# Kernel optimization log

Hardware: AMD Instinct MI355X
Metric: run time of the kernel (lower is better)

Reference implementation:

```python
import jax, jax.numpy as jnp
import numpy as np

T, H, I, E, Z = 4096, 1024, 512, 64, 16   # tokens, hidden, intermediate, routed experts, zero experts
TOP_K = 2
SCALE = 1.5        # routed_scaling_factor
CAP = 320


def setup_inputs() -> dict:
    key = jax.random.key(0)
    k1, k2, k3, k4, k5 = jax.random.split(key, 5)
    return {
        "hidden_states": jax.random.normal(k1, (T, H), dtype=jnp.float32),
        "router_w": jax.random.normal(k2, (E + Z, H), dtype=jnp.float32) * 0.02,
        "correction_bias": jnp.zeros((E + Z,), dtype=jnp.float32),
        "w_gate": jax.random.normal(k3, (E, H, I), dtype=jnp.float32) * 0.02,
        "w_up": jax.random.normal(k4, (E, H, I), dtype=jnp.float32) * 0.02,
        "w_down": jax.random.normal(k5, (E, I, H), dtype=jnp.float32) * 0.02,
    }


def _moe_forward(hidden_states, router_w, correction_bias, w_gate, w_up, w_down):
    n_tok = hidden_states.shape[0]
    # ---- Router (fp32 gemm) ----
    logits = hidden_states @ router_w.T                      # [T, E+Z]
    scores = jax.nn.sigmoid(logits)                          # DeepSeek-V3-style sigmoid gating
    biased = scores + correction_bias[None, :]
    _, top_idx = jax.lax.top_k(biased, TOP_K)                # [T, K] selection on biased scores
    top_w = jnp.take_along_axis(scores, top_idx, axis=-1)    # weights from unbiased scores, no renorm

    # ---- Zero (identity) experts: ids >= E return the input token ----
    is_zero = top_idx >= E                                   # [T, K]
    zero_out = (top_w * is_zero).sum(-1, keepdims=True) * hidden_states

    # ---- Routed expert dispatch (capacity-based grouped GEMM) ----
    flat_e = jnp.where(is_zero, 0, top_idx).reshape(-1)      # [T*K]
    flat_w = jnp.where(is_zero, 0.0, top_w).reshape(-1)      # [T*K]
    routed_mask = (~is_zero).reshape(-1)
    oh = jax.nn.one_hot(flat_e, E, dtype=jnp.int32) * routed_mask[:, None].astype(jnp.int32)
    pos = (jnp.cumsum(oh, axis=0) * oh).sum(-1) - 1          # rank within expert; -1 for zero-expert slots
    valid = (pos >= 0) & (pos < CAP)
    pos_c = jnp.where(valid, pos, CAP)                       # overflow/zero slots -> spill row CAP
    x_rep = jnp.repeat(hidden_states, TOP_K, axis=0)         # [T*K, H]
    buf = jnp.zeros((E, CAP + 1, hidden_states.shape[1]), dtype=hidden_states.dtype)
    buf = buf.at[flat_e, pos_c].set(x_rep)[:, :CAP]          # [E, CAP, H]

    # ---- Grouped SwiGLU experts ----
    g = jax.nn.silu(jnp.einsum('ech,ehi->eci', buf, w_gate)) * jnp.einsum('ech,ehi->eci', buf, w_up)
    out_e = jnp.einsum('eci,eih->ech', g, w_down)            # [E, CAP, H]

    # ---- Combine ----
    pos_g = jnp.where(valid, pos, 0)
    y = out_e[flat_e, pos_g] * (flat_w * valid)[:, None]     # [T*K, H]
    routed = y.reshape(n_tok, TOP_K, -1).sum(1)

    return (routed + zero_out) * SCALE                       # routed_scaling_factor applied on output


def reference(hidden_states, router_w, correction_bias, w_gate, w_up, w_down):
    return _moe_forward(hidden_states, router_w, correction_bias, w_gate, w_up, w_down)
```

## Files before the change

### kernel.cpp

```cpp
#include <hip/hip_runtime.h>
#include <hip/hip_bf16.h>
#include <stdint.h>


#define T_TOK 4096
#define HDIM  1024
#define IDIM  512
#define NE    64
#define NEZ   80
#define CAPE  320
#define SCALEF 1.5f

typedef __attribute__((ext_vector_type(8))) short bf16x8;
typedef __attribute__((ext_vector_type(4))) float floatx4;

static __device__ __forceinline__ unsigned short f2bf(float f) {
    unsigned int x = __float_as_uint(f);
    x += 0x7fffu + ((x >> 16) & 1u);
    return (unsigned short)(x >> 16);
}
static __device__ __forceinline__ float bf2f(unsigned short u) {
    return __uint_as_float(((unsigned int)u) << 16);
}
static __device__ __forceinline__ uint4 pack8(const float* f) {
    uint4 v;
    asm("v_cvt_pk_bf16_f32 %0, %1, %2" : "=v"(v.x) : "v"(f[0]), "v"(f[1]));
    asm("v_cvt_pk_bf16_f32 %0, %1, %2" : "=v"(v.y) : "v"(f[2]), "v"(f[3]));
    asm("v_cvt_pk_bf16_f32 %0, %1, %2" : "=v"(v.z) : "v"(f[4]), "v"(f[5]));
    asm("v_cvt_pk_bf16_f32 %0, %1, %2" : "=v"(v.w) : "v"(f[6]), "v"(f[7]));
    return v;
}
static __device__ __forceinline__ uint2 pack4(float4 f) {
    uint2 v;
    asm("v_cvt_pk_bf16_f32 %0, %1, %2" : "=v"(v.x) : "v"(f.x), "v"(f.y));
    asm("v_cvt_pk_bf16_f32 %0, %1, %2" : "=v"(v.y) : "v"(f.z), "v"(f.w));
    return v;
}

__global__ __launch_bounds__(256) void router_kernel(
    const float* __restrict__ hidden, const float* __restrict__ rw,
    const float* __restrict__ bias, int* __restrict__ cnt,
    int* __restrict__ slot_tok, float* __restrict__ w_routed,
    float* __restrict__ zc)
{
    __shared__ float sc[8][NEZ];
    __shared__ float sbias[NEZ];
    const int tid = threadIdx.x;
    const int w = tid >> 6, lane = tid & 63;
    const int t0 = blockIdx.x * 8 + w * 2;

    if (tid < NEZ) sbias[tid] = bias[tid];

    float4 xr[2][4];
#pragma unroll
    for (int tt = 0; tt < 2; ++tt)
#pragma unroll
        for (int j4 = 0; j4 < 4; ++j4)
            xr[tt][j4] = *(const float4*)&hidden[(size_t)(t0 + tt) * HDIM + lane * 16 + j4 * 4];

    for (int eb = 0; eb < NEZ; eb += 16) {
        float acc[2][16];
#pragma unroll
        for (int tt = 0; tt < 2; ++tt)
#pragma unroll
            for (int ee = 0; ee < 16; ++ee) acc[tt][ee] = 0.f;

#pragma unroll
        for (int ee = 0; ee < 16; ++ee) {
            const float* r = rw + (size_t)(eb + ee) * HDIM + lane * 16;
#pragma unroll
            for (int j4 = 0; j4 < 4; ++j4) {
                float4 rv = *(const float4*)&r[j4 * 4];
                acc[0][ee] += xr[0][j4].x * rv.x + xr[0][j4].y * rv.y
                            + xr[0][j4].z * rv.z + xr[0][j4].w * rv.w;
                acc[1][ee] += xr[1][j4].x * rv.x + xr[1][j4].y * rv.y
                            + xr[1][j4].z * rv.z + xr[1][j4].w * rv.w;
            }
        }
#pragma unroll
        for (int off = 32; off > 0; off >>= 1)
#pragma unroll
            for (int tt = 0; tt < 2; ++tt)
#pragma unroll
                for (int ee = 0; ee < 16; ++ee)
                    acc[tt][ee] += __shfl_xor(acc[tt][ee], off);

        if (lane == 0) {
#pragma unroll
            for (int tt = 0; tt < 2; ++tt)
#pragma unroll
                for (int ee = 0; ee < 16; ++ee)
                    sc[w * 2 + tt][eb + ee] = 1.f / (1.f + __expf(-acc[tt][ee]));
        }
    }
    __syncthreads();

    if (tid < 8) {
        const int t = blockIdx.x * 8 + tid;
        float b1 = -1e30f, b2 = -1e30f; int i1 = 0, i2 = 0;
        for (int e = 0; e < NEZ; ++e) {
            float b = sc[tid][e] + sbias[e];
            if (b > b1) { b2 = b1; i2 = i1; b1 = b; i1 = e; }
            else if (b > b2) { b2 = b; i2 = e; }
        }
        float z = 0.f;
        int idx2[2] = { i1, i2 };
        for (int k = 0; k < 2; ++k) {
            int e = idx2[k];
            float wgt = sc[tid][e];
            float wr = 0.f;
            if (e >= NE) {
                z += wgt;
            } else {
                int pos = atomicAdd(&cnt[e], 1);
                if (pos < CAPE) { slot_tok[e * CAPE + pos] = t * 2 + k; wr = wgt; }
            }
            w_routed[t * 2 + k] = wr;
        }
        zc[t] = z;
    }
}

#define GU_BG 2048
#define GU_BU 4096
__global__ __launch_bounds__(256, 4) void gateup_kernel(
    const float* __restrict__ hidden,
    const float* __restrict__ w_gate, const float* __restrict__ w_up,
    const int* __restrict__ cnt, const int* __restrict__ slot_tok,
    unsigned short* __restrict__ gbuf)
{
    const int e  = blockIdx.x;
    const int n0 = blockIdx.y * 64;
    const int m0 = blockIdx.z * 64;
    int cnt_e = cnt[e]; if (cnt_e > CAPE) cnt_e = CAPE;
    if (m0 >= cnt_e) return;

    __shared__ unsigned short lds[6144];
    __shared__ int sTok[64];

    const int tid = threadIdx.x;
    const int lane = tid & 63, wid = tid >> 6;
    const int ml = lane & 15, quad = lane >> 4;
    const int wm = wid >> 1, wn = wid & 1;

    if (tid < 64) {
        int r = m0 + tid;
        sTok[tid] = (r < cnt_e) ? (slot_tok[e * CAPE + r] >> 1) : 0;
    }
    __syncthreads();

    const int ak4 = tid & 7;
    const float* ha[2];
    int aoff[2];
#pragma unroll
    for (int p = 0; p < 2; ++p) {
        int arow = (tid >> 3) + 32 * p;
        aoff[p] = (arow >> 4) * 512 + ((ak4 >> 1) * 16 + (arow & 15)) * 8 + (ak4 & 1) * 4;
        ha[p] = hidden + (size_t)sTok[arow] * HDIM + ak4 * 4;
    }
    const int bn = tid & 63, bq = tid >> 6;
    const int boff = (bn >> 4) * 512 + (bq * 16 + (bn & 15)) * 8;

    const size_t ebase = (size_t)e * HDIM * IDIM;
    const float* wg_p = w_gate + ebase + (size_t)(bq * 8) * IDIM + n0 + bn;
    const float* wu_p = w_up   + ebase + (size_t)(bq * 8) * IDIM + n0 + bn;

    float4 aR[2];
    float  gR[8], uR[8];

#pragma unroll
    for (int p = 0; p < 2; ++p) aR[p] = *(const float4*)ha[p];
#pragma unroll
    for (int jj = 0; jj < 8; ++jj) {
        gR[jj] = wg_p[(size_t)jj * IDIM];
        uR[jj] = wu_p[(size_t)jj * IDIM];
    }

    floatx4 ag[2][2], au[2][2];
#pragma unroll
    for (int mt = 0; mt < 2; ++mt)
#pragma unroll
        for (int nt = 0; nt < 2; ++nt) {
            ag[mt][nt] = (floatx4){0.f, 0.f, 0.f, 0.f};
            au[mt][nt] = (floatx4){0.f, 0.f, 0.f, 0.f};
        }

    for (int kc = 0; kc < HDIM; kc += 32) {
        {
#pragma unroll
            for (int p = 0; p < 2; ++p)
                *(uint2*)&lds[aoff[p]] = pack4(aR[p]);
            *(uint4*)&lds[GU_BG + boff] = pack8(gR);
            *(uint4*)&lds[GU_BU + boff] = pack8(uR);
        }
        __syncthreads();

        if (kc + 32 < HDIM) {
            wg_p += (size_t)32 * IDIM; wu_p += (size_t)32 * IDIM;
#pragma unroll
            for (int p = 0; p < 2; ++p) { ha[p] += 32; aR[p] = *(const float4*)ha[p]; }
#pragma unroll
            for (int jj = 0; jj < 8; ++jj) {
                gR[jj] = wg_p[(size_t)jj * IDIM];
                uR[jj] = wu_p[(size_t)jj * IDIM];
            }
        }

        bf16x8 a[2], bg[2], bu[2];
#pragma unroll
        for (int mt = 0; mt < 2; ++mt)
            a[mt] = *(const bf16x8*)&lds[(wm * 2 + mt) * 512 + lane * 8];
#pragma unroll
        for (int nt = 0; nt < 2; ++nt) {
            bg[nt] = *(const bf16x8*)&lds[GU_BG + (wn * 2 + nt) * 512 + lane * 8];
            bu[nt] = *(const bf16x8*)&lds[GU_BU + (wn * 2 + nt) * 512 + lane * 8];
        }
#pragma unroll
        for (int mt = 0; mt < 2; ++mt)
#pragma unroll
            for (int nt = 0; nt < 2; ++nt) {
                ag[mt][nt] = __builtin_amdgcn_mfma_f32_16x16x32_bf16(a[mt], bg[nt], ag[mt][nt], 0, 0, 0);
                au[mt][nt] = __builtin_amdgcn_mfma_f32_16x16x32_bf16(a[mt], bu[nt], au[mt][nt], 0, 0, 0);
            }
        __syncthreads();
    }

#pragma unroll
    for (int mt = 0; mt < 2; ++mt) {
#pragma unroll
        for (int r4 = 0; r4 < 4; ++r4) {
            int gm = m0 + wm * 32 + mt * 16 + quad * 4 + r4;
            if (gm < cnt_e) {
                unsigned short* grow = gbuf + (size_t)(e * CAPE + gm) * IDIM + n0 + wn * 32;
#pragma unroll
                for (int nt = 0; nt < 2; ++nt) {
                    float g = ag[mt][nt][r4];
                    float u = au[mt][nt][r4];
                    float s = g / (1.f + __expf(-g));
                    grow[nt * 16 + ml] = f2bf(s * u);
                }
            }
        }
    }
}

#define DN_B 2048
__global__ __launch_bounds__(256, 4) void down_kernel(
    const unsigned short* __restrict__ gbuf, const float* __restrict__ w_down,
    const int* __restrict__ cnt, const int* __restrict__ slot_tok,
    unsigned short* __restrict__ y2)
{
    const int e  = blockIdx.x;
    const int n0 = blockIdx.y * 128;
    const int m0 = blockIdx.z * 64;
    int cnt_e = cnt[e]; if (cnt_e > CAPE) cnt_e = CAPE;
    if (m0 >= cnt_e) return;

    __shared__ unsigned short lds[6144];
    __shared__ int sSlot[64];

    const int tid = threadIdx.x;
    const int lane = tid & 63, wid = tid >> 6;
    const int ml = lane & 15, quad = lane >> 4;
    const int wm = wid >> 1, wn = wid & 1;

    if (tid < 64) {
        int r = m0 + tid;
        sSlot[tid] = (r < cnt_e) ? slot_tok[e * CAPE + r] : 0;
    }
    __syncthreads();

    const int arow = tid >> 2, au8 = tid & 3;
    const int aoff = (arow >> 4) * 512 + (au8 * 16 + (arow & 15)) * 8;
    const unsigned short* gp = gbuf + (size_t)(e * CAPE + m0 + arow) * IDIM + au8 * 8;
    const int bn = tid & 127, bk = tid >> 7;
    const int boff0 = (bn >> 4) * 512 + ((bk * 2) * 16 + (bn & 15)) * 8;
    const int boff1 = boff0 + 128;
    const float* wd_p = w_down + (size_t)e * IDIM * HDIM + (size_t)(bk * 16) * HDIM + n0 + bn;

    uint4 aR;
    float bR[16];

    aR = *(const uint4*)gp;
#pragma unroll
    for (int jj = 0; jj < 16; ++jj) bR[jj] = wd_p[(size_t)jj * HDIM];

    floatx4 acc[2][4];
#pragma unroll
    for (int mt = 0; mt < 2; ++mt)
#pragma unroll
        for (int nt = 0; nt < 4; ++nt)
            acc[mt][nt] = (floatx4){0.f, 0.f, 0.f, 0.f};

    for (int kc = 0; kc < IDIM; kc += 32) {
        *(uint4*)&lds[aoff] = aR;
        *(uint4*)&lds[DN_B + boff0] = pack8(bR);
        *(uint4*)&lds[DN_B + boff1] = pack8(bR + 8);
        __syncthreads();

        if (kc + 32 < IDIM) {
            gp += 32;
            wd_p += (size_t)32 * HDIM;
            aR = *(const uint4*)gp;
#pragma unroll
            for (int jj = 0; jj < 16; ++jj) bR[jj] = wd_p[(size_t)jj * HDIM];
        }

        bf16x8 a[2], b[4];
#pragma unroll
        for (int mt = 0; mt < 2; ++mt)
            a[mt] = *(const bf16x8*)&lds[(wm * 2 + mt) * 512 + lane * 8];
#pragma unroll
        for (int nt = 0; nt < 4; ++nt)
            b[nt] = *(const bf16x8*)&lds[DN_B + (wn * 4 + nt) * 512 + lane * 8];
#pragma unroll
        for (int mt = 0; mt < 2; ++mt)
#pragma unroll
            for (int nt = 0; nt < 4; ++nt)
                acc[mt][nt] = __builtin_amdgcn_mfma_f32_16x16x32_bf16(a[mt], b[nt], acc[mt][nt], 0, 0, 0);
        __syncthreads();
    }

#pragma unroll
    for (int mt = 0; mt < 2; ++mt) {
#pragma unroll
        for (int r4 = 0; r4 < 4; ++r4) {
            int lrow = wm * 32 + mt * 16 + quad * 4 + r4;
            if (m0 + lrow < cnt_e) {
                int slot = sSlot[lrow];
                unsigned short* yrow = y2 + (size_t)slot * HDIM + n0 + wn * 64;
#pragma unroll
                for (int nt = 0; nt < 4; ++nt)
                    yrow[nt * 16 + ml] = f2bf(acc[mt][nt][r4]);
            }
        }
    }
}

__global__ __launch_bounds__(256) void combine_kernel(
    const float* __restrict__ hidden, const unsigned short* __restrict__ y2,
    const float* __restrict__ w_routed, const float* __restrict__ zc,
    float* __restrict__ out)
{
    int gid = blockIdx.x * 256 + threadIdx.x;
    int t = gid >> 8;
    int h = (gid & 255) * 4;
    float4 x = *(const float4*)(hidden + (size_t)t * HDIM + h);
    float w0 = w_routed[t * 2 + 0];
    float w1 = w_routed[t * 2 + 1];
    float z  = zc[t];
    ushort4 ya = *(const ushort4*)(y2 + (size_t)(t * 2 + 0) * HDIM + h);
    ushort4 yb = *(const ushort4*)(y2 + (size_t)(t * 2 + 1) * HDIM + h);
    float4 o;
    o.x = SCALEF * (z * x.x + w0 * bf2f(ya.x) + w1 * bf2f(yb.x));
    o.y = SCALEF * (z * x.y + w0 * bf2f(ya.y) + w1 * bf2f(yb.y));
    o.z = SCALEF * (z * x.z + w0 * bf2f(ya.z) + w1 * bf2f(yb.z));
    o.w = SCALEF * (z * x.w + w0 * bf2f(ya.w) + w1 * bf2f(yb.w));
    *(float4*)(out + (size_t)t * HDIM + h) = o;
}

#define OFF_CNT   0
#define OFF_SLOT  4096
#define OFF_WR    (OFF_SLOT + NE * CAPE * 4)
#define OFF_ZC    (OFF_WR + T_TOK * 2 * 4)
#define OFF_GBUF  (OFF_ZC + T_TOK * 4)
#define OFF_Y2    (OFF_GBUF + (size_t)NE * CAPE * IDIM * 2)

extern "C" void kernel_launch(void* const* d_in, const int* in_sizes, int n_in,
                              void* d_out, int out_size, void* d_ws, size_t ws_size,
                              hipStream_t stream) {
    const float* hidden = (const float*)d_in[0];
    const float* rw     = (const float*)d_in[1];
    const float* bias   = (const float*)d_in[2];
    const float* w_gate = (const float*)d_in[3];
    const float* w_up   = (const float*)d_in[4];
    const float* w_down = (const float*)d_in[5];
    float* out = (float*)d_out;

    char* ws = (char*)d_ws;
    int*   cnt      = (int*)(ws + OFF_CNT);
    int*   slot_tok = (int*)(ws + OFF_SLOT);
    float* w_rt     = (float*)(ws + OFF_WR);
    float* zc       = (float*)(ws + OFF_ZC);
    unsigned short* gbuf = (unsigned short*)(ws + OFF_GBUF);
    unsigned short* y2   = (unsigned short*)(ws + OFF_Y2);

    hipMemsetAsync(cnt, 0, NE * sizeof(int), stream);

    router_kernel<<<T_TOK / 8, 256, 0, stream>>>(hidden, rw, bias, cnt, slot_tok, w_rt, zc);

    gateup_kernel<<<dim3(NE, IDIM / 64, CAPE / 64), 256, 0, stream>>>(
        hidden, w_gate, w_up, cnt, slot_tok, gbuf);

    down_kernel<<<dim3(NE, HDIM / 128, CAPE / 64), 256, 0, stream>>>(
        gbuf, w_down, cnt, slot_tok, y2);

    combine_kernel<<<(T_TOK * HDIM / 4) / 256, 256, 0, stream>>>(
        hidden, y2, w_rt, zc, out);
}
```

Before: 484.8 us.

## Widen gate/up N-tile to 128 and restructure router to 16 lanes per token

The gate/up kernel now computes a 64x128 output tile per block instead of 64x64. Each gathered hidden-state tile is reused across twice as many weight columns, and the number of blocks that re-read activations is halved. Launch bounds drop to 2 blocks per SM and LDS and register use grow, which may reduce occupancy. Separately, the router now assigns 16 lanes per token and 16 tokens per block, using a shorter shuffle reduction, so router weights are read once per 16 tokens instead of once per 8.

```diff
diff --git a/kernel.cpp b/kernel.cpp
--- a/kernel.cpp
+++ b/kernel.cpp
@@ -43,60 +43,50 @@
     int* __restrict__ slot_tok, float* __restrict__ w_routed,
     float* __restrict__ zc)
 {
-    __shared__ float sc[8][NEZ];
+    __shared__ float sc[16][NEZ];
     __shared__ float sbias[NEZ];
     const int tid = threadIdx.x;
     const int w = tid >> 6, lane = tid & 63;
-    const int t0 = blockIdx.x * 8 + w * 2;
+    const int g = lane >> 4, s = lane & 15;
+    const int t = blockIdx.x * 16 + w * 4 + g;
 
     if (tid < NEZ) sbias[tid] = bias[tid];
 
-    float4 xr[2][4];
-#pragma unroll
-    for (int tt = 0; tt < 2; ++tt)
-#pragma unroll
-        for (int j4 = 0; j4 < 4; ++j4)
-            xr[tt][j4] = *(const float4*)&hidden[(size_t)(t0 + tt) * HDIM + lane * 16 + j4 * 4];
-
-    for (int eb = 0; eb < NEZ; eb += 16) {
-        float acc[2][16];
-#pragma unroll
-        for (int tt = 0; tt < 2; ++tt)
-#pragma unroll
-            for (int ee = 0; ee < 16; ++ee) acc[tt][ee] = 0.f;
-
-#pragma unroll
-        for (int ee = 0; ee < 16; ++ee) {
-            const float* r = rw + (size_t)(eb + ee) * HDIM + lane * 16;
-#pragma unroll
-            for (int j4 = 0; j4 < 4; ++j4) {
-                float4 rv = *(const float4*)&r[j4 * 4];
-                acc[0][ee] += xr[0][j4].x * rv.x + xr[0][j4].y * rv.y
-                            + xr[0][j4].z * rv.z + xr[0][j4].w * rv.w;
-                acc[1][ee] += xr[1][j4].x * rv.x + xr[1][j4].y * rv.y
-                            + xr[1][j4].z * rv.z + xr[1][j4].w * rv.w;
-            }
-        }
-#pragma unroll
-        for (int off = 32; off > 0; off >>= 1)
-#pragma unroll
-            for (int tt = 0; tt < 2; ++tt)
-#pragma unroll
-                for (int ee = 0; ee < 16; ++ee)
-                    acc[tt][ee] += __shfl_xor(acc[tt][ee], off);
-
-        if (lane == 0) {
-#pragma unroll
-            for (int tt = 0; tt < 2; ++tt)
-#pragma unroll
-                for (int ee = 0; ee < 16; ++ee)
-                    sc[w * 2 + tt][eb + ee] = 1.f / (1.f + __expf(-acc[tt][ee]));
+    float4 xr[16];
+#pragma unroll
+    for (int j = 0; j < 16; ++j)
+        xr[j] = *(const float4*)&hidden[(size_t)t * HDIM + j * 64 + s * 4];
+
+    for (int eb = 0; eb < NEZ; eb += 8) {
+        float acc[8];
+#pragma unroll
+        for (int i = 0; i < 8; ++i) acc[i] = 0.f;
+
+#pragma unroll
+        for (int j = 0; j < 16; ++j) {
+#pragma unroll
+            for (int i = 0; i < 8; ++i) {
+                float4 rv = *(const float4*)&rw[(size_t)(eb + i) * HDIM + j * 64 + s * 4];
+                acc[i] += xr[j].x * rv.x + xr[j].y * rv.y
+                        + xr[j].z * rv.z + xr[j].w * rv.w;
+            }
+        }
+#pragma unroll
+        for (int off = 8; off > 0; off >>= 1)
+#pragma unroll
+            for (int i = 0; i < 8; ++i)
+                acc[i] += __shfl_xor(acc[i], off);
+
+        if (s == 0) {
+#pragma unroll
+            for (int i = 0; i < 8; ++i)
+                sc[w * 4 + g][eb + i] = 1.f / (1.f + __expf(-acc[i]));
         }
     }
     __syncthreads();
 
-    if (tid < 8) {
-        const int t = blockIdx.x * 8 + tid;
+    if (tid < 16) {
+        const int t2 = blockIdx.x * 16 + tid;
         float b1 = -1e30f, b2 = -1e30f; int i1 = 0, i2 = 0;
         for (int e = 0; e < NEZ; ++e) {
             float b = sc[tid][e] + sbias[e];
@@ -113,29 +103,29 @@
                 z += wgt;
             } else {
                 int pos = atomicAdd(&cnt[e], 1);
-                if (pos < CAPE) { slot_tok[e * CAPE + pos] = t * 2 + k; wr = wgt; }
-            }
-            w_routed[t * 2 + k] = wr;
-        }
-        zc[t] = z;
+                if (pos < CAPE) { slot_tok[e * CAPE + pos] = t2 * 2 + k; wr = wgt; }
+            }
+            w_routed[t2 * 2 + k] = wr;
+        }
+        zc[t2] = z;
     }
 }
 
 #define GU_BG 2048
-#define GU_BU 4096
-__global__ __launch_bounds__(256, 4) void gateup_kernel(
+#define GU_BU 6144
+__global__ __launch_bounds__(256, 2) void gateup_kernel(
     const float* __restrict__ hidden,
     const float* __restrict__ w_gate, const float* __restrict__ w_up,
     const int* __restrict__ cnt, const int* __restrict__ slot_tok,
     unsigned short* __restrict__ gbuf)
 {
     const int e  = blockIdx.x;
-    const int n0 = blockIdx.y * 64;
+    const int n0 = blockIdx.y * 128;
     const int m0 = blockIdx.z * 64;
     int cnt_e = cnt[e]; if (cnt_e > CAPE) cnt_e = CAPE;
     if (m0 >= cnt_e) return;
 
-    __shared__ unsigned short lds[6144];
+    __shared__ unsigned short lds[10240];
     __shared__ int sTok[64];
 
     const int tid = threadIdx.x;
@@ -149,76 +139,76 @@
     }
     __syncthreads();
 
-    const int ak4 = tid & 7;
-    const float* ha[2];
-    int aoff[2];
-#pragma unroll
-    for (int p = 0; p < 2; ++p) {
-        int arow = (tid >> 3) + 32 * p;
-        aoff[p] = (arow >> 4) * 512 + ((ak4 >> 1) * 16 + (arow & 15)) * 8 + (ak4 & 1) * 4;
-        ha[p] = hidden + (size_t)sTok[arow] * HDIM + ak4 * 4;
-    }
-    const int bn = tid & 63, bq = tid >> 6;
-    const int boff = (bn >> 4) * 512 + (bq * 16 + (bn & 15)) * 8;
+    const int arow0 = tid >> 3, ak4 = tid & 7;
+    const int aoff0 = (arow0 >> 4) * 512 + ((ak4 >> 1) * 16 + (arow0 & 15)) * 8 + (ak4 & 1) * 4;
+    const int arow1 = arow0 + 32;
+    const int aoff1 = (arow1 >> 4) * 512 + ((ak4 >> 1) * 16 + (arow1 & 15)) * 8 + (ak4 & 1) * 4;
+    const int bn = tid & 127, bk = tid >> 7;
+    const int boff0 = (bn >> 4) * 512 + ((bk * 2) * 16 + (bn & 15)) * 8;
+    const int boff1 = boff0 + 128;
 
     const size_t ebase = (size_t)e * HDIM * IDIM;
-    const float* wg_p = w_gate + ebase + (size_t)(bq * 8) * IDIM + n0 + bn;
-    const float* wu_p = w_up   + ebase + (size_t)(bq * 8) * IDIM + n0 + bn;
+    const float* wg_p = w_gate + ebase + (size_t)(bk * 16) * IDIM + n0 + bn;
+    const float* wu_p = w_up   + ebase + (size_t)(bk * 16) * IDIM + n0 + bn;
+    const float* ha0 = hidden + (size_t)sTok[arow0] * HDIM + ak4 * 4;
+    const float* ha1 = hidden + (size_t)sTok[arow1] * HDIM + ak4 * 4;
 
     float4 aR[2];
-    float  gR[8], uR[8];
-
-#pragma unroll
-    for (int p = 0; p < 2; ++p) aR[p] = *(const float4*)ha[p];
-#pragma unroll
-    for (int jj = 0; jj < 8; ++jj) {
+    float  gR[16], uR[16];
+
+    aR[0] = *(const float4*)ha0;
+    aR[1] = *(const float4*)ha1;
+#pragma unroll
+    for (int jj = 0; jj < 16; ++jj) {
         gR[jj] = wg_p[(size_t)jj * IDIM];
         uR[jj] = wu_p[(size_t)jj * IDIM];
     }
 
-    floatx4 ag[2][2], au[2][2];
+    floatx4 ag[2][4], au[2][4];
 #pragma unroll
     for (int mt = 0; mt < 2; ++mt)
 #pragma unroll
-        for (int nt = 0; nt < 2; ++nt) {
+        for (int nt = 0; nt < 4; ++nt) {
             ag[mt][nt] = (floatx4){0.f, 0.f, 0.f, 0.f};
             au[mt][nt] = (floatx4){0.f, 0.f, 0.f, 0.f};
         }
 
     for (int kc = 0; kc < HDIM; kc += 32) {
         {
-#pragma unroll
-            for (int p = 0; p < 2; ++p)
-                *(uint2*)&lds[aoff[p]] = pack4(aR[p]);
-            *(uint4*)&lds[GU_BG + boff] = pack8(gR);
-            *(uint4*)&lds[GU_BU + boff] = pack8(uR);
+            *(uint2*)&lds[aoff0] = pack4(aR[0]);
+            *(uint2*)&lds[aoff1] = pack4(aR[1]);
+            *(uint4*)&lds[GU_BG + boff0] = pack8(gR);
+            *(uint4*)&lds[GU_BG + boff1] = pack8(gR + 8);
+            *(uint4*)&lds[GU_BU + boff0] = pack8(uR);
+            *(uint4*)&lds[GU_BU + boff1] = pack8(uR + 8);
         }
         __syncthreads();
 
         if (kc + 32 < HDIM) {
+            ha0 += 32; ha1 += 32;
             wg_p += (size_t)32 * IDIM; wu_p += (size_t)32 * IDIM;
-#pragma unroll
-            for (int p = 0; p < 2; ++p) { ha[p] += 32; aR[p] = *(const float4*)ha[p]; }
-#pragma unroll
-            for (int jj = 0; jj < 8; ++jj) {
+            aR[0] = *(const float4*)ha0;
+            aR[1] = *(const float4*)ha1;
+#pragma unroll
+            for (int jj = 0; jj < 16; ++jj) {
                 gR[jj] = wg_p[(size_t)jj * IDIM];
                 uR[jj] = wu_p[(size_t)jj * IDIM];
             }
         }
 
-        bf16x8 a[2], bg[2], bu[2];
+        bf16x8 a[2], bg[4], bu[4];
 #pragma unroll
         for (int mt = 0; mt < 2; ++mt)
             a[mt] = *(const bf16x8*)&lds[(wm * 2 + mt) * 512 + lane * 8];
 #pragma unroll
-        for (int nt = 0; nt < 2; ++nt) {
-            bg[nt] = *(const bf16x8*)&lds[GU_BG + (wn * 2 + nt) * 512 + lane * 8];
-            bu[nt] = *(const bf16x8*)&lds[GU_BU + (wn * 2 + nt) * 512 + lane * 8];
+        for (int nt = 0; nt < 4; ++nt) {
+            bg[nt] = *(const bf16x8*)&lds[GU_BG + (wn * 4 + nt) * 512 + lane * 8];
+            bu[nt] = *(const bf16x8*)&lds[GU_BU + (wn * 4 + nt) * 512 + lane * 8];
         }
 #pragma unroll
         for (int mt = 0; mt < 2; ++mt)
 #pragma unroll
-            for (int nt = 0; nt < 2; ++nt) {
+            for (int nt = 0; nt < 4; ++nt) {
                 ag[mt][nt] = __builtin_amdgcn_mfma_f32_16x16x32_bf16(a[mt], bg[nt], ag[mt][nt], 0, 0, 0);
                 au[mt][nt] = __builtin_amdgcn_mfma_f32_16x16x32_bf16(a[mt], bu[nt], au[mt][nt], 0, 0, 0);
             }
@@ -231,9 +221,9 @@
         for (int r4 = 0; r4 < 4; ++r4) {
             int gm = m0 + wm * 32 + mt * 16 + quad * 4 + r4;
             if (gm < cnt_e) {
-                unsigned short* grow = gbuf + (size_t)(e * CAPE + gm) * IDIM + n0 + wn * 32;
-#pragma unroll
-                for (int nt = 0; nt < 2; ++nt) {
+                unsigned short* grow = gbuf + (size_t)(e * CAPE + gm) * IDIM + n0 + wn * 64;
+#pragma unroll
+                for (int nt = 0; nt < 4; ++nt) {
                     float g = ag[mt][nt][r4];
                     float u = au[mt][nt][r4];
                     float s = g / (1.f + __expf(-g));
@@ -387,9 +377,9 @@
 
     hipMemsetAsync(cnt, 0, NE * sizeof(int), stream);
 
-    router_kernel<<<T_TOK / 8, 256, 0, stream>>>(hidden, rw, bias, cnt, slot_tok, w_rt, zc);
-
-    gateup_kernel<<<dim3(NE, IDIM / 64, CAPE / 64), 256, 0, stream>>>(
+    router_kernel<<<T_TOK / 16, 256, 0, stream>>>(hidden, rw, bias, cnt, slot_tok, w_rt, zc);
+
+    gateup_kernel<<<dim3(NE, IDIM / 128, CAPE / 64), 256, 0, stream>>>(
         hidden, w_gate, w_up, cnt, slot_tok, gbuf);
 
     down_kernel<<<dim3(NE, HDIM / 128, CAPE / 64), 256, 0, stream>>>(
```

New measurement: 528.2 us. +8.9%, slower.
